# Kernel optimization log

Hardware: AMD Instinct MI355X
Metric: run time of the kernel (lower is better)

## Reference

```python
import jax, jax.numpy as jnp
import numpy as np

# Scaled-down LLaMA-style decoder with per-layer memory K/V prefix (tokenmix2 Decoder)
L, D, H, Dh, F, V = 2, 4096, 32, 128, 8192, 8192
B, S, M = 1, 1024, 512
EPS = 1e-5
ROPE_BASE = 10000.0


def setup_inputs() -> dict:
    key = jax.random.key(0)
    ks = jax.random.split(key, 16)
    sd = D ** -0.5
    sf = F ** -0.5
    n = lambda k, shape, s: (jax.random.normal(k, shape, jnp.float32) * s)
    return {
        "input_ids": jax.random.randint(ks[0], (B, S), 0, V),
        "memory": jax.random.normal(ks[1], (L, B, M, D), jnp.float32),
        "embed": n(ks[2], (V, D), sd),
        "Wq": n(ks[3], (L, D, D), sd),
        "Wk": n(ks[4], (L, D, D), sd),
        "Wv": n(ks[5], (L, D, D), sd),
        "Wo": n(ks[6], (L, D, D), sd),
        "Wg": n(ks[7], (L, F, D), sd),
        "Wu": n(ks[8], (L, F, D), sd),
        "Wd": n(ks[9], (L, D, F), sf),
        "Wmk": n(ks[10], (L, D, D), sd),
        "Wmv": n(ks[11], (L, D, D), sd),
        "ln1": jnp.ones((L, D), jnp.float32),
        "ln2": jnp.ones((L, D), jnp.float32),
        "normw": jnp.ones((D,), jnp.float32),
        "lm_head": n(ks[12], (V, D), sd),
    }


def _rms(x, w):
    return x * jax.lax.rsqrt(jnp.mean(x * x, axis=-1, keepdims=True) + EPS) * w


def _rot_half(x):
    x1, x2 = jnp.split(x, 2, axis=-1)
    return jnp.concatenate([-x2, x1], axis=-1)


def _rope_tables(n_pos):
    inv_freq = 1.0 / (ROPE_BASE ** (jnp.arange(0, Dh, 2, dtype=jnp.float32) / Dh))
    ang = jnp.arange(n_pos, dtype=jnp.float32)[:, None] * inv_freq[None, :]
    emb = jnp.concatenate([ang, ang], axis=-1)  # [n_pos, Dh]
    return jnp.cos(emb), jnp.sin(emb)


def reference(input_ids, memory, embed, Wq, Wk, Wv, Wo, Wg, Wu, Wd, Wmk, Wmv,
              ln1, ln2, normw, lm_head):
    h = embed[input_ids]                                   # [B,S,D]
    cos, sin = _rope_tables(M + S)                         # memory tokens sit at positions 0..M
    cos_k, sin_k = cos[None, None], sin[None, None]        # [1,1,M+S,Dh]
    cos_q, sin_q = cos[None, None, M:], sin[None, None, M:]  # queries at positions M..M+S
    qpos = jnp.arange(M, M + S)
    kpos = jnp.arange(M + S)
    mask = qpos[:, None] >= kpos[None, :]                  # causal incl. full memory prefix
    scale = Dh ** -0.5

    def heads(x, T):
        return x.reshape(B, T, H, Dh).transpose(0, 2, 1, 3)  # [B,H,T,Dh]

    for l in range(L):
        x = _rms(h, ln1[l])
        q = heads(x @ Wq[l].T, S)
        k = heads(x @ Wk[l].T, S)
        v = heads(x @ Wv[l].T, S)
        mk = heads(memory[l] @ Wmk[l].T, M)
        mv = heads(memory[l] @ Wmv[l].T, M)
        K = jnp.concatenate([mk, k], axis=2)               # [B,H,M+S,Dh]
        Vv = jnp.concatenate([mv, v], axis=2)
        q = q * cos_q + _rot_half(q) * sin_q
        K = K * cos_k + _rot_half(K) * sin_k
        scores = jnp.einsum('bhqd,bhkd->bhqk', q, K) * scale
        scores = jnp.where(mask, scores, jnp.float32(-1e30))
        p = jax.nn.softmax(scores, axis=-1)
        o = jnp.einsum('bhqk,bhkd->bhqd', p, Vv)
        o = o.transpose(0, 2, 1, 3).reshape(B, S, D)
        h = h + o @ Wo[l].T
        x = _rms(h, ln2[l])
        h = h + (jax.nn.silu(x @ Wg[l].T) * (x @ Wu[l].T)) @ Wd[l].T

    h = _rms(h, normw)
    logits = (h @ lm_head.T).astype(jnp.float32)           # [B,S,V]
    return logits
```

## Files before the change

kernel.cpp:

```cpp
#include <hip/hip_runtime.h>
#include <hip/hip_bf16.h>

typedef unsigned int uint;
typedef unsigned short u16;

#define D_ 4096
#define H_ 32
#define DH 128
#define F_ 8192
#define V_ 8192
#define S_ 1024
#define M_ 512
#define L_ 2
#define KV_ (M_ + S_)

typedef __attribute__((ext_vector_type(8))) short s16x8;
typedef __attribute__((ext_vector_type(4))) float f32x4;
typedef __attribute__((ext_vector_type(4))) u16 u16x4;

__device__ __forceinline__ u16 f2bf(float f) {
    uint u = __float_as_uint(f);
    u += 0x7FFFu + ((u >> 16) & 1u);
    return (u16)(u >> 16);
}
__device__ __forceinline__ float bf2f(u16 h) {
    return __uint_as_float(((uint)h) << 16);
}
__device__ __forceinline__ uint cvt_pk_bf16(float a, float b) {
    uint r;
    asm volatile("v_cvt_pk_bf16_f32 %0, %1, %2" : "=v"(r) : "v"(a), "v"(b));
    return r;
}
__device__ __forceinline__ void gload_lds16(const void* g, void* l) {
    __builtin_amdgcn_global_load_lds(
        (const __attribute__((address_space(1))) unsigned int*)g,
        (__attribute__((address_space(3))) unsigned int*)l, 16, 0, 0);
}

__global__ void k_embed(const int* __restrict__ ids, const float* __restrict__ embed,
                        float* __restrict__ h) {
    int row = blockIdx.x;
    const float4* src = (const float4*)(embed + (size_t)ids[row] * D_);
    float4* dst = (float4*)(h + (size_t)row * D_);
    for (int i = threadIdx.x; i < D_ / 4; i += 256) dst[i] = src[i];
}

__global__ __launch_bounds__(256) void k_rms(const float* __restrict__ hin,
                                             const float* __restrict__ w,
                                             u16* __restrict__ out) {
    int row = blockIdx.x, t = threadIdx.x;
    const float4* src = (const float4*)(hin + (size_t)row * D_);
    float4 v[4];
    float ss = 0.f;
#pragma unroll
    for (int i = 0; i < 4; ++i) {
        v[i] = src[t + 256 * i];
        ss += v[i].x * v[i].x + v[i].y * v[i].y + v[i].z * v[i].z + v[i].w * v[i].w;
    }
#pragma unroll
    for (int off = 32; off; off >>= 1) ss += __shfl_xor(ss, off);
    __shared__ float red[4];
    if ((t & 63) == 0) red[t >> 6] = ss;
    __syncthreads();
    float tot = red[0] + red[1] + red[2] + red[3];
    float sc = rsqrtf(tot * (1.0f / D_) + 1e-5f);
    const float4* wp = (const float4*)w;
    u16x4* op = (u16x4*)(out + (size_t)row * D_);
#pragma unroll
    for (int i = 0; i < 4; ++i) {
        float4 wv = wp[t + 256 * i];
        u16x4 o;
        o[0] = f2bf(v[i].x * sc * wv.x);
        o[1] = f2bf(v[i].y * sc * wv.y);
        o[2] = f2bf(v[i].z * sc * wv.z);
        o[3] = f2bf(v[i].w * sc * wv.w);
        op[t + 256 * i] = o;
    }
}

__global__ void k_cvt(const float* __restrict__ src, u16* __restrict__ dst, int n4) {
    int i = blockIdx.x * 256 + threadIdx.x;
    if (i < n4) {
        float4 v = ((const float4*)src)[i];
        u16x4 o;
        o[0] = f2bf(v.x); o[1] = f2bf(v.y); o[2] = f2bf(v.z); o[3] = f2bf(v.w);
        ((u16x4*)dst)[i] = o;
    }
}

__global__ void k_ropetab(float* __restrict__ tab) {
    int pos = blockIdx.x, i = threadIdx.x;
    float invf = powf(10000.0f, -(float)i * (1.0f / 64.0f));
    float ang = (float)pos * invf;
    tab[(size_t)pos * 128 + i * 2] = cosf(ang);
    tab[(size_t)pos * 128 + i * 2 + 1] = sinf(ang);
}

__global__ __launch_bounds__(256) void k_rope(u16* __restrict__ buf,
                                              const float* __restrict__ tab, int pos0) {
    int row = blockIdx.x, t = threadIdx.x;
    const float2* tp = (const float2*)(tab + (size_t)(pos0 + row) * 128);
    u16* p = buf + (size_t)row * D_;
#pragma unroll
    for (int j = 0; j < 8; ++j) {
        int pid = t + 256 * j;
        int hd = pid >> 6, i = pid & 63;
        float2 cs = tp[i];
        int base = hd * 128 + i;
        float v0 = bf2f(p[base]), v1 = bf2f(p[base + 64]);
        p[base] = f2bf(v0 * cs.x - v1 * cs.y);
        p[base + 64] = f2bf(v1 * cs.x + v0 * cs.y);
    }
}

__global__ __launch_bounds__(256) void k_transpose(const u16* __restrict__ src,
                                                   u16* __restrict__ dst) {
    __shared__ u16 tile[64][66];
    int tc = blockIdx.x * 64;
    int tr = blockIdx.y * 64;
    int t = threadIdx.x;
    int c = t & 63, r0 = t >> 6;
#pragma unroll
    for (int i = 0; i < 16; ++i) {
        int r = r0 + i * 4;
        tile[r][c] = src[(size_t)(tr + r) * D_ + tc + c];
    }
    __syncthreads();
#pragma unroll
    for (int i = 0; i < 16; ++i) {
        int r = r0 + i * 4;
        dst[(size_t)(tc + r) * KV_ + tr + c] = tile[c][r];
    }
}

struct GemmBatch {
    const u16* A[5];
    const float* B[5];
    void* O[5];
    int mrows[5];
    int koff[5];
    float* aux;
};

template <int EPI>
__global__ __launch_bounds__(256) void k_gemm(GemmBatch P, int Nn, int Kstep, int Kfull) {
    int z = blockIdx.z;
    size_t bm = blockIdx.y, bn = blockIdx.x;
    if ((int)(bm * 128) >= P.mrows[z]) return;
    const u16* A = P.A[z];
    const float* Bw = P.B[z];
    int koff = P.koff[z];

    __shared__ __align__(16) u16 As[128 * 64];
    __shared__ __align__(16) u16 Bs[128 * 64];
    int tid = threadIdx.x;
    int lane = tid & 63, wid = tid >> 6;
    int l16 = lane & 15, lh = lane >> 4;
    int wm = (wid >> 1) * 64, wn = (wid & 1) * 64;

    const u16* pA[4];
    const float* pB[4];
    int ldsAo[4], bso[4];
#pragma unroll
    for (int i = 0; i < 4; ++i) {
        int c = tid + 256 * i;
        int r = c >> 3, s = c & 7;
        pA[i] = A + (size_t)(bm * 128 + r) * Kfull + koff + s * 8;
        pB[i] = Bw + (size_t)(bn * 128 + r) * Kfull + koff + s * 8;
        ldsAo[i] = c * 8;
        bso[i] = r * 64 + ((s ^ (r & 7)) * 8);
    }

    f32x4 acc[4][4];
#pragma unroll
    for (int i = 0; i < 4; ++i)
#pragma unroll
        for (int j = 0; j < 4; ++j)
#pragma unroll
            for (int e = 0; e < 4; ++e) acc[i][j][e] = 0.f;

    float4 br[8];
    auto issueA = [&](int k0) {
#pragma unroll
        for (int i = 0; i < 4; ++i)
            gload_lds16(pA[i] + k0, &As[0] + ldsAo[i]);
    };
    auto loadB = [&](int k0) {
#pragma unroll
        for (int i = 0; i < 4; ++i) {
            br[2 * i] = *(const float4*)(pB[i] + k0);
            br[2 * i + 1] = *(const float4*)(pB[i] + k0 + 4);
        }
    };
    auto cvtwriteB = [&]() {
#pragma unroll
        for (int i = 0; i < 4; ++i) {
            uint4 w;
            w.x = cvt_pk_bf16(br[2 * i].x, br[2 * i].y);
            w.y = cvt_pk_bf16(br[2 * i].z, br[2 * i].w);
            w.z = cvt_pk_bf16(br[2 * i + 1].x, br[2 * i + 1].y);
            w.w = cvt_pk_bf16(br[2 * i + 1].z, br[2 * i + 1].w);
            *(uint4*)(&Bs[bso[i]]) = w;
        }
    };
    auto compute = [&]() {
#pragma unroll
        for (int kk = 0; kk < 2; ++kk) {
            int sidx = kk * 4 + lh;
            s16x8 af[4], bf4[4];
#pragma unroll
            for (int mi = 0; mi < 4; ++mi)
                af[mi] = *(const s16x8*)(&As[(wm + mi * 16 + l16) * 64 + sidx * 8]);
#pragma unroll
            for (int ni = 0; ni < 4; ++ni) {
                int r = wn + ni * 16 + l16;
                bf4[ni] = *(const s16x8*)(&Bs[r * 64 + ((sidx ^ (r & 7)) * 8)]);
            }
#pragma unroll
            for (int mi = 0; mi < 4; ++mi)
#pragma unroll
                for (int ni = 0; ni < 4; ++ni)
                    acc[mi][ni] = __builtin_amdgcn_mfma_f32_16x16x32_bf16(
                        af[mi], bf4[ni], acc[mi][ni], 0, 0, 0);
        }
    };

    int nt = Kstep >> 6;
    loadB(0);
    for (int t = 0; t < nt; ++t) {
        issueA(t << 6);
        cvtwriteB();
        if (t + 1 < nt) loadB((t + 1) << 6);
        __syncthreads();
        compute();
        __syncthreads();
    }

    void* Oo = P.O[z];
#pragma unroll
    for (int mi = 0; mi < 4; ++mi) {
#pragma unroll
        for (int ni = 0; ni < 4; ++ni) {
#pragma unroll
            for (int r = 0; r < 4; ++r) {
                int grow = (int)bm * 128 + wm + mi * 16 + lh * 4 + r;
                int gcol = (int)bn * 128 + wn + ni * 16 + l16;
                size_t idx = (size_t)grow * Nn + gcol;
                float v = acc[mi][ni][r];
                if constexpr (EPI == 0) {
                    ((u16*)Oo)[idx] = f2bf(v);
                } else if constexpr (EPI == 1) {
                    ((float*)Oo)[idx] = v;
                } else if constexpr (EPI == 3) {
                    float g = P.aux[idx];
                    float sg = g / (1.0f + __expf(-g));
                    ((u16*)Oo)[idx] = f2bf(sg * v);
                } else {
                    atomicAdd((float*)Oo + idx, v);
                }
            }
        }
    }
}

__global__ __launch_bounds__(64) void k_attn(const u16* __restrict__ Qb,
                                             const u16* __restrict__ Kb,
                                             const u16* __restrict__ VT,
                                             u16* __restrict__ Ob) {
    int qt = blockIdx.x, hd = blockIdx.y;
    int lane = threadIdx.x, l16 = lane & 15, lh = lane >> 4;
    __shared__ __align__(16) float Pl[16 * 36];

    s16x8 qf[4];
#pragma unroll
    for (int c = 0; c < 4; ++c)
        qf[c] = *(const s16x8*)(Qb + (size_t)(qt * 16 + l16) * D_ + hd * DH + c * 32 + lh * 8);

    f32x4 o[8];
#pragma unroll
    for (int dc = 0; dc < 8; ++dc)
#pragma unroll
        for (int e = 0; e < 4; ++e) o[dc][e] = 0.f;
    float m[4], lsum[4];
#pragma unroll
    for (int r = 0; r < 4; ++r) { m[r] = -1e30f; lsum[r] = 0.f; }

    const float scale = 0.08838834764831845f;
    int qbase = M_ + qt * 16;
    int nkb = (M_ + qt * 16 + 16 + 31) >> 5;

    for (int kb = 0; kb < nkb; ++kb) {
        f32x4 s0, s1;
#pragma unroll
        for (int e = 0; e < 4; ++e) { s0[e] = 0.f; s1[e] = 0.f; }
#pragma unroll
        for (int c = 0; c < 4; ++c) {
            s16x8 kf0 = *(const s16x8*)(Kb + (size_t)(kb * 32 + l16) * D_ + hd * DH + c * 32 + lh * 8);
            s16x8 kf1 = *(const s16x8*)(Kb + (size_t)(kb * 32 + 16 + l16) * D_ + hd * DH + c * 32 + lh * 8);
            s0 = __builtin_amdgcn_mfma_f32_16x16x32_bf16(qf[c], kf0, s0, 0, 0, 0);
            s1 = __builtin_amdgcn_mfma_f32_16x16x32_bf16(qf[c], kf1, s1, 0, 0, 0);
        }
        int kp0 = kb * 32 + l16, kp1 = kp0 + 16;
        float pm[4];
#pragma unroll
        for (int r = 0; r < 4; ++r) {
            int qp = qbase + lh * 4 + r;
            float v0 = s0[r] * scale; if (kp0 > qp) v0 = -1e30f;
            float v1 = s1[r] * scale; if (kp1 > qp) v1 = -1e30f;
            s0[r] = v0; s1[r] = v1;
            pm[r] = fmaxf(v0, v1);
        }
#pragma unroll
        for (int r = 0; r < 4; ++r) {
#pragma unroll
            for (int off = 8; off; off >>= 1) pm[r] = fmaxf(pm[r], __shfl_xor(pm[r], off));
        }
        float alpha[4];
#pragma unroll
        for (int r = 0; r < 4; ++r) {
            float mn = fmaxf(m[r], pm[r]);
            alpha[r] = __expf(m[r] - mn);
            m[r] = mn;
            float p0 = __expf(s0[r] - mn), p1 = __expf(s1[r] - mn);
            s0[r] = p0; s1[r] = p1;
            float t = p0 + p1;
#pragma unroll
            for (int off = 8; off; off >>= 1) t += __shfl_xor(t, off);
            lsum[r] = lsum[r] * alpha[r] + t;
        }
#pragma unroll
        for (int r = 0; r < 4; ++r) {
            Pl[(lh * 4 + r) * 36 + l16] = s0[r];
            Pl[(lh * 4 + r) * 36 + 16 + l16] = s1[r];
        }
        __syncthreads();
        s16x8 pf;
        {
            const f32x4* pp = (const f32x4*)(Pl + l16 * 36 + lh * 8);
            f32x4 a = pp[0], b = pp[1];
            pf[0] = (short)f2bf(a[0]); pf[1] = (short)f2bf(a[1]);
            pf[2] = (short)f2bf(a[2]); pf[3] = (short)f2bf(a[3]);
            pf[4] = (short)f2bf(b[0]); pf[5] = (short)f2bf(b[1]);
            pf[6] = (short)f2bf(b[2]); pf[7] = (short)f2bf(b[3]);
        }
        __syncthreads();
#pragma unroll
        for (int dc = 0; dc < 8; ++dc) {
#pragma unroll
            for (int r = 0; r < 4; ++r) o[dc][r] *= alpha[r];
        }
#pragma unroll
        for (int dc = 0; dc < 8; ++dc) {
            s16x8 vf = *(const s16x8*)(VT + (size_t)(hd * DH + dc * 16 + l16) * KV_ + kb * 32 + lh * 8);
            o[dc] = __builtin_amdgcn_mfma_f32_16x16x32_bf16(pf, vf, o[dc], 0, 0, 0);
        }
    }
#pragma unroll
    for (int dc = 0; dc < 8; ++dc) {
#pragma unroll
        for (int r = 0; r < 4; ++r) {
            float val = o[dc][r] / lsum[r];
            Ob[(size_t)(qt * 16 + lh * 4 + r) * D_ + hd * DH + dc * 16 + l16] = f2bf(val);
        }
    }
}

extern "C" void kernel_launch(void* const* d_in, const int* in_sizes, int n_in,
                              void* d_out, int out_size, void* d_ws, size_t ws_size,
                              hipStream_t stream) {
    const int* ids = (const int*)d_in[0];
    const float* memory = (const float*)d_in[1];
    const float* embed = (const float*)d_in[2];
    const float* Wq = (const float*)d_in[3];
    const float* Wk = (const float*)d_in[4];
    const float* Wv = (const float*)d_in[5];
    const float* Wo = (const float*)d_in[6];
    const float* Wg = (const float*)d_in[7];
    const float* Wu = (const float*)d_in[8];
    const float* Wd = (const float*)d_in[9];
    const float* Wmk = (const float*)d_in[10];
    const float* Wmv = (const float*)d_in[11];
    const float* ln1 = (const float*)d_in[12];
    const float* ln2 = (const float*)d_in[13];
    const float* normw = (const float*)d_in[14];
    const float* lm = (const float*)d_in[15];

    char* ws = (char*)d_ws;
    float* h   = (float*)(ws + 0x0000000);
    u16* xb    = (u16*)(ws + 0x1000000);
    float* tab = (float*)(ws + 0x1800000);
    u16* memb  = (u16*)(ws + 0x1900000);
    u16* Qb    = (u16*)(ws + 0x1E00000);
    u16* Kb    = (u16*)(ws + 0x2600000);
    u16* Vb    = (u16*)(ws + 0x3200000);
    u16* VT    = (u16*)(ws + 0x3E00000);
    u16* Ob    = (u16*)(ws + 0x4A00000);
    float* Gbuf = (float*)(ws + 0x1E00000);
    u16* tb     = (u16*)(ws + 0x3E00000);

    k_embed<<<S_, 256, 0, stream>>>(ids, embed, h);
    k_ropetab<<<KV_, 64, 0, stream>>>(tab);

    for (int l = 0; l < L_; ++l) {
        const float* Wq_l = Wq + (size_t)l * D_ * D_;
        const float* Wk_l = Wk + (size_t)l * D_ * D_;
        const float* Wv_l = Wv + (size_t)l * D_ * D_;
        const float* Wo_l = Wo + (size_t)l * D_ * D_;
        const float* Wmk_l = Wmk + (size_t)l * D_ * D_;
        const float* Wmv_l = Wmv + (size_t)l * D_ * D_;
        const float* Wg_l = Wg + (size_t)l * (size_t)F_ * D_;
        const float* Wu_l = Wu + (size_t)l * (size_t)F_ * D_;
        const float* Wd_l = Wd + (size_t)l * (size_t)D_ * F_;

        k_rms<<<S_, 256, 0, stream>>>(h, ln1 + l * D_, xb);
        k_cvt<<<(M_ * D_ / 4 + 255) / 256, 256, 0, stream>>>(
            memory + (size_t)l * M_ * D_, memb, M_ * D_ / 4);

        GemmBatch g1{};
        g1.A[0] = xb;   g1.B[0] = Wq_l;  g1.O[0] = Qb;                    g1.mrows[0] = S_;
        g1.A[1] = xb;   g1.B[1] = Wk_l;  g1.O[1] = Kb + (size_t)M_ * D_;  g1.mrows[1] = S_;
        g1.A[2] = xb;   g1.B[2] = Wv_l;  g1.O[2] = Vb + (size_t)M_ * D_;  g1.mrows[2] = S_;
        g1.A[3] = memb; g1.B[3] = Wmk_l; g1.O[3] = Kb;                    g1.mrows[3] = M_;
        g1.A[4] = memb; g1.B[4] = Wmv_l; g1.O[4] = Vb;                    g1.mrows[4] = M_;
        k_gemm<0><<<dim3(D_ / 128, S_ / 128, 5), 256, 0, stream>>>(g1, D_, D_, D_);

        k_rope<<<S_, 256, 0, stream>>>(Qb, tab, M_);
        k_rope<<<KV_, 256, 0, stream>>>(Kb, tab, 0);
        k_transpose<<<dim3(D_ / 64, KV_ / 64), 256, 0, stream>>>(Vb, VT);
        k_attn<<<dim3(S_ / 16, H_), 64, 0, stream>>>(Qb, Kb, VT, Ob);

        GemmBatch g2{};
        g2.A[0] = Ob; g2.B[0] = Wo_l; g2.O[0] = h; g2.mrows[0] = S_; g2.koff[0] = 0;
        g2.A[1] = Ob; g2.B[1] = Wo_l; g2.O[1] = h; g2.mrows[1] = S_; g2.koff[1] = 2048;
        k_gemm<4><<<dim3(D_ / 128, S_ / 128, 2), 256, 0, stream>>>(g2, D_, 2048, D_);

        k_rms<<<S_, 256, 0, stream>>>(h, ln2 + l * D_, xb);
        GemmBatch g3{};
        g3.A[0] = xb; g3.B[0] = Wg_l; g3.O[0] = Gbuf; g3.mrows[0] = S_;
        k_gemm<1><<<dim3(F_ / 128, S_ / 128, 1), 256, 0, stream>>>(g3, F_, D_, D_);
        GemmBatch g4{};
        g4.A[0] = xb; g4.B[0] = Wu_l; g4.O[0] = tb; g4.mrows[0] = S_; g4.aux = Gbuf;
        k_gemm<3><<<dim3(F_ / 128, S_ / 128, 1), 256, 0, stream>>>(g4, F_, D_, D_);
        GemmBatch g5{};
        g5.A[0] = tb; g5.B[0] = Wd_l; g5.O[0] = h; g5.mrows[0] = S_; g5.koff[0] = 0;
        g5.A[1] = tb; g5.B[1] = Wd_l; g5.O[1] = h; g5.mrows[1] = S_; g5.koff[1] = 4096;
        k_gemm<4><<<dim3(D_ / 128, S_ / 128, 2), 256, 0, stream>>>(g5, D_, 4096, F_);
    }

    k_rms<<<S_, 256, 0, stream>>>(h, normw, xb);
    GemmBatch g6{};
    g6.A[0] = xb; g6.B[0] = lm; g6.O[0] = (float*)d_out; g6.mrows[0] = S_;
    k_gemm<1><<<dim3(V_ / 128, S_ / 128, 1), 256, 0, stream>>>(g6, V_, D_, D_);
}
```

Baseline: 1.891 ms.

## Preconvert weights to bf16 and add pipelined 256x256 GEMM kernel

All fp32 weight matrices are converted to bf16 in workspace at the start of each call, so GEMMs load both operands directly into LDS with async loads instead of converting B tiles in registers. A new 512-thread 256x256 tile GEMM with double-buffered LDS, staggered prefetch and priority hints handles the QKV/memory projections and a batched gate/up projection. The SiLU epilogue moves to a separate elementwise kernel, and split-K atomic accumulation is replaced by single-pass read-add-write. This adds extra conversion traffic every call and drops the LDS swizzle, which may raise bank conflicts.

Measured after the change: 2.618 ms. 38.5% more time.

```diff
diff --git a/kernel.cpp b/kernel.cpp
--- a/kernel.cpp
+++ b/kernel.cpp
@@ -26,11 +26,6 @@
 __device__ __forceinline__ float bf2f(u16 h) {
     return __uint_as_float(((uint)h) << 16);
 }
-__device__ __forceinline__ uint cvt_pk_bf16(float a, float b) {
-    uint r;
-    asm volatile("v_cvt_pk_bf16_f32 %0, %1, %2" : "=v"(r) : "v"(a), "v"(b));
-    return r;
-}
 __device__ __forceinline__ void gload_lds16(const void* g, void* l) {
     __builtin_amdgcn_global_load_lds(
         (const __attribute__((address_space(1))) unsigned int*)g,
@@ -88,6 +83,21 @@
     }
 }
 
+__global__ void k_silu(const float* __restrict__ G, const float* __restrict__ U,
+                       u16* __restrict__ out, int n4) {
+    int i = blockIdx.x * 256 + threadIdx.x;
+    if (i < n4) {
+        float4 g = ((const float4*)G)[i];
+        float4 u = ((const float4*)U)[i];
+        u16x4 o;
+        o[0] = f2bf(g.x / (1.0f + __expf(-g.x)) * u.x);
+        o[1] = f2bf(g.y / (1.0f + __expf(-g.y)) * u.y);
+        o[2] = f2bf(g.z / (1.0f + __expf(-g.z)) * u.z);
+        o[3] = f2bf(g.w / (1.0f + __expf(-g.w)) * u.w);
+        ((u16x4*)out)[i] = o;
+    }
+}
+
 __global__ void k_ropetab(float* __restrict__ tab) {
     int pos = blockIdx.x, i = threadIdx.x;
     float invf = powf(10000.0f, -(float)i * (1.0f / 64.0f));
@@ -133,24 +143,138 @@
     }
 }
 
-struct GemmBatch {
+struct GemmB8 {
     const u16* A[5];
-    const float* B[5];
+    const u16* B[5];
     void* O[5];
     int mrows[5];
-    int koff[5];
-    float* aux;
 };
 
 template <int EPI>
-__global__ __launch_bounds__(256) void k_gemm(GemmBatch P, int Nn, int Kstep, int Kfull) {
+__global__ __launch_bounds__(512, 2) void k_gemm8(GemmB8 P, int Nn, int Kfull) {
+    int z = blockIdx.z;
+    size_t bm = blockIdx.y, bn = blockIdx.x;
+    if ((int)(bm * 256) >= P.mrows[z]) return;
+    const u16* A = P.A[z];
+    const u16* Bw = P.B[z];
+    __shared__ __align__(16) u16 AB[2][2][2][128][64];
+
+    const int tid = threadIdx.x;
+    const int lane = tid & 63, wid = tid >> 6;
+    const int l16 = lane & 15, lh = lane >> 4;
+    const int wrow = (wid >> 2) * 64;
+    const int wcol = (wid & 3) * 32;
+    const int nt = Kfull >> 6;
+
+    const int grow0 = tid >> 3;
+    const int gcol0 = (tid & 7) * 8;
+    const u16* pA = A + (size_t)(bm * 256 + grow0) * Kfull + gcol0;
+    const u16* pB = Bw + (size_t)(bn * 256 + grow0) * Kfull + gcol0;
+
+    auto stage = [&](const u16* base, int mat, int h, int t) {
+        if (t >= nt) return;
+        const u16* g = base + (size_t)(h * 128) * Kfull + t * 64;
+        u16* l = &AB[t & 1][mat][h][0][0] + tid * 8;
+        gload_lds16(g, l);
+        gload_lds16(g + (size_t)64 * Kfull, l + 4096);
+    };
+
+    f32x4 acc[4][4][2];
+#pragma unroll
+    for (int q = 0; q < 4; ++q)
+#pragma unroll
+        for (int mf = 0; mf < 4; ++mf)
+#pragma unroll
+            for (int nf = 0; nf < 2; ++nf)
+#pragma unroll
+                for (int e = 0; e < 4; ++e) acc[q][mf][nf][e] = 0.f;
+
+    stage(pA, 0, 0, 0); stage(pB, 1, 0, 0);
+    stage(pA, 0, 1, 0); stage(pB, 1, 1, 0);
+    stage(pA, 0, 0, 1); stage(pB, 1, 0, 1);
+    asm volatile("s_waitcnt vmcnt(4)" ::: "memory");
+    __builtin_amdgcn_s_barrier();
+    asm volatile("" ::: "memory");
+
+    for (int T = 0; T < nt; ++T) {
+        const int cb = T & 1;
+#pragma unroll
+        for (int q = 0; q < 4; ++q) {
+            const int qm = q >> 1, qn = q & 1;
+            s16x8 af[4][2], bb[2][2];
+#pragma unroll
+            for (int kk = 0; kk < 2; ++kk) {
+                const int co = (kk * 4 + lh) * 8;
+#pragma unroll
+                for (int mf = 0; mf < 4; ++mf)
+                    af[mf][kk] = *(const s16x8*)(&AB[cb][0][qm][wrow + mf * 16 + l16][co]);
+#pragma unroll
+                for (int nf = 0; nf < 2; ++nf)
+                    bb[nf][kk] = *(const s16x8*)(&AB[cb][1][qn][wcol + nf * 16 + l16][co]);
+            }
+            if (q == 0) stage(pA, 0, 1, T + 1);
+            else if (q == 1) stage(pB, 1, 1, T + 1);
+            else if (q == 2) stage(pA, 0, 0, T + 2);
+            else stage(pB, 1, 0, T + 2);
+            asm volatile("" ::: "memory");
+            __builtin_amdgcn_s_barrier();
+            asm volatile("" ::: "memory");
+            __builtin_amdgcn_s_setprio(1);
+#pragma unroll
+            for (int kk = 0; kk < 2; ++kk)
+#pragma unroll
+                for (int mf = 0; mf < 4; ++mf)
+#pragma unroll
+                    for (int nf = 0; nf < 2; ++nf)
+                        acc[q][mf][nf] = __builtin_amdgcn_mfma_f32_16x16x32_bf16(
+                            af[mf][kk], bb[nf][kk], acc[q][mf][nf], 0, 0, 0);
+            __builtin_amdgcn_s_setprio(0);
+            if (q == 3) {
+                if (T < nt - 2) asm volatile("s_waitcnt vmcnt(4)" ::: "memory");
+                else if (T == nt - 2) asm volatile("s_waitcnt vmcnt(0)" ::: "memory");
+            }
+            asm volatile("" ::: "memory");
+            __builtin_amdgcn_s_barrier();
+            asm volatile("" ::: "memory");
+        }
+    }
+
+    void* Oo = P.O[z];
+#pragma unroll
+    for (int q = 0; q < 4; ++q) {
+        const int qm = q >> 1, qn = q & 1;
+#pragma unroll
+        for (int mf = 0; mf < 4; ++mf) {
+#pragma unroll
+            for (int nf = 0; nf < 2; ++nf) {
+#pragma unroll
+                for (int rr = 0; rr < 4; ++rr) {
+                    int grow = (int)bm * 256 + qm * 128 + wrow + mf * 16 + lh * 4 + rr;
+                    int gcol = (int)bn * 256 + qn * 128 + wcol + nf * 16 + l16;
+                    size_t idx = (size_t)grow * Nn + gcol;
+                    float v = acc[q][mf][nf][rr];
+                    if constexpr (EPI == 0) ((u16*)Oo)[idx] = f2bf(v);
+                    else ((float*)Oo)[idx] = v;
+                }
+            }
+        }
+    }
+}
+
+struct GemmB2 {
+    const u16* A[5];
+    const u16* B[5];
+    void* O[5];
+    int mrows[5];
+};
+
+template <int EPI>
+__global__ __launch_bounds__(256) void k_gemm2(GemmB2 P, int Nn, int Kfull) {
     int z = blockIdx.z;
     size_t bm = blockIdx.y, bn = blockIdx.x;
     if ((int)(bm * 128) >= P.mrows[z]) return;
     const u16* A = P.A[z];
-    const float* Bw = P.B[z];
-    int koff = P.koff[z];
-
+    const u16* Bw = P.B[z];
     __shared__ __align__(16) u16 As[128 * 64];
     __shared__ __align__(16) u16 Bs[128 * 64];
     int tid = threadIdx.x;
@@ -158,17 +282,15 @@
     int l16 = lane & 15, lh = lane >> 4;
     int wm = (wid >> 1) * 64, wn = (wid & 1) * 64;
 
-    const u16* pA[4];
-    const float* pB[4];
-    int ldsAo[4], bso[4];
+    const u16 *pA[4], *pB[4];
+    int ldso[4];
 #pragma unroll
     for (int i = 0; i < 4; ++i) {
         int c = tid + 256 * i;
         int r = c >> 3, s = c & 7;
-        pA[i] = A + (size_t)(bm * 128 + r) * Kfull + koff + s * 8;
-        pB[i] = Bw + (size_t)(bn * 128 + r) * Kfull + koff + s * 8;
-        ldsAo[i] = c * 8;
-        bso[i] = r * 64 + ((s ^ (r & 7)) * 8);
+        pA[i] = A + (size_t)(bm * 128 + r) * Kfull + s * 8;
+        pB[i] = Bw + (size_t)(bn * 128 + r) * Kfull + s * 8;
+        ldso[i] = c * 8;
     }
 
     f32x4 acc[4][4];
@@ -179,31 +301,14 @@
 #pragma unroll
             for (int e = 0; e < 4; ++e) acc[i][j][e] = 0.f;
 
-    float4 br[8];
-    auto issueA = [&](int k0) {
-#pragma unroll
-        for (int i = 0; i < 4; ++i)
-            gload_lds16(pA[i] + k0, &As[0] + ldsAo[i]);
-    };
-    auto loadB = [&](int k0) {
-#pragma unroll
-        for (int i = 0; i < 4; ++i) {
-            br[2 * i] = *(const float4*)(pB[i] + k0);
-            br[2 * i + 1] = *(const float4*)(pB[i] + k0 + 4);
-        }
-    };
-    auto cvtwriteB = [&]() {
-#pragma unroll
-        for (int i = 0; i < 4; ++i) {
-            uint4 w;
-            w.x = cvt_pk_bf16(br[2 * i].x, br[2 * i].y);
-            w.y = cvt_pk_bf16(br[2 * i].z, br[2 * i].w);
-            w.z = cvt_pk_bf16(br[2 * i + 1].x, br[2 * i + 1].y);
-            w.w = cvt_pk_bf16(br[2 * i + 1].z, br[2 * i + 1].w);
-            *(uint4*)(&Bs[bso[i]]) = w;
-        }
-    };
-    auto compute = [&]() {
+    int nt = Kfull >> 6;
+    for (int t = 0; t < nt; ++t) {
+        int k0 = t << 6;
+#pragma unroll
+        for (int i = 0; i < 4; ++i) gload_lds16(pA[i] + k0, &As[ldso[i]]);
+#pragma unroll
+        for (int i = 0; i < 4; ++i) gload_lds16(pB[i] + k0, &Bs[ldso[i]]);
+        __syncthreads();
 #pragma unroll
         for (int kk = 0; kk < 2; ++kk) {
             int sidx = kk * 4 + lh;
@@ -212,10 +317,8 @@
             for (int mi = 0; mi < 4; ++mi)
                 af[mi] = *(const s16x8*)(&As[(wm + mi * 16 + l16) * 64 + sidx * 8]);
 #pragma unroll
-            for (int ni = 0; ni < 4; ++ni) {
-                int r = wn + ni * 16 + l16;
-                bf4[ni] = *(const s16x8*)(&Bs[r * 64 + ((sidx ^ (r & 7)) * 8)]);
-            }
+            for (int ni = 0; ni < 4; ++ni)
+                bf4[ni] = *(const s16x8*)(&Bs[(wn + ni * 16 + l16) * 64 + sidx * 8]);
 #pragma unroll
             for (int mi = 0; mi < 4; ++mi)
 #pragma unroll
@@ -223,16 +326,6 @@
                     acc[mi][ni] = __builtin_amdgcn_mfma_f32_16x16x32_bf16(
                         af[mi], bf4[ni], acc[mi][ni], 0, 0, 0);
         }
-    };
-
-    int nt = Kstep >> 6;
-    loadB(0);
-    for (int t = 0; t < nt; ++t) {
-        issueA(t << 6);
-        cvtwriteB();
-        if (t + 1 < nt) loadB((t + 1) << 6);
-        __syncthreads();
-        compute();
         __syncthreads();
     }
 
@@ -247,17 +340,8 @@
                 int gcol = (int)bn * 128 + wn + ni * 16 + l16;
                 size_t idx = (size_t)grow * Nn + gcol;
                 float v = acc[mi][ni][r];
-                if constexpr (EPI == 0) {
-                    ((u16*)Oo)[idx] = f2bf(v);
-                } else if constexpr (EPI == 1) {
-                    ((float*)Oo)[idx] = v;
-                } else if constexpr (EPI == 3) {
-                    float g = P.aux[idx];
-                    float sg = g / (1.0f + __expf(-g));
-                    ((u16*)Oo)[idx] = f2bf(sg * v);
-                } else {
-                    atomicAdd((float*)Oo + idx, v);
-                }
+                if constexpr (EPI == 1) ((float*)Oo)[idx] = v;
+                else ((float*)Oo)[idx] += v;
             }
         }
     }
@@ -397,58 +481,71 @@
     u16* Ob    = (u16*)(ws + 0x4A00000);
     float* Gbuf = (float*)(ws + 0x1E00000);
     u16* tb     = (u16*)(ws + 0x3E00000);
+    float* Ubuf = (float*)(ws + 0x4E00000);
+    u16* Wqb  = (u16*)(ws + 0x07000000);
+    u16* Wkb  = (u16*)(ws + 0x0B000000);
+    u16* Wvb  = (u16*)(ws + 0x0F000000);
+    u16* Wob  = (u16*)(ws + 0x13000000);
+    u16* Wmkb = (u16*)(ws + 0x17000000);
+    u16* Wmvb = (u16*)(ws + 0x1B000000);
+    u16* Wgb  = (u16*)(ws + 0x1F000000);
+    u16* Wub  = (u16*)(ws + 0x27000000);
+    u16* Wdb  = (u16*)(ws + 0x2F000000);
+    u16* lmb  = (u16*)(ws + 0x37000000);
+
+    const int nDD = L_ * D_ * D_ / 4, nFD = L_ * F_ * D_ / 4, nVD = V_ * D_ / 4;
+    k_cvt<<<(nDD + 255) / 256, 256, 0, stream>>>(Wq, Wqb, nDD);
+    k_cvt<<<(nDD + 255) / 256, 256, 0, stream>>>(Wk, Wkb, nDD);
+    k_cvt<<<(nDD + 255) / 256, 256, 0, stream>>>(Wv, Wvb, nDD);
+    k_cvt<<<(nDD + 255) / 256, 256, 0, stream>>>(Wo, Wob, nDD);
+    k_cvt<<<(nDD + 255) / 256, 256, 0, stream>>>(Wmk, Wmkb, nDD);
+    k_cvt<<<(nDD + 255) / 256, 256, 0, stream>>>(Wmv, Wmvb, nDD);
+    k_cvt<<<(nFD + 255) / 256, 256, 0, stream>>>(Wg, Wgb, nFD);
+    k_cvt<<<(nFD + 255) / 256, 256, 0, stream>>>(Wu, Wub, nFD);
+    k_cvt<<<(nFD + 255) / 256, 256, 0, stream>>>(Wd, Wdb, nFD);
+    k_cvt<<<(nVD + 255) / 256, 256, 0, stream>>>(lm, lmb, nVD);
 
     k_embed<<<S_, 256, 0, stream>>>(ids, embed, h);
     k_ropetab<<<KV_, 64, 0, stream>>>(tab);
 
     for (int l = 0; l < L_; ++l) {
-        const float* Wq_l = Wq + (size_t)l * D_ * D_;
-        const float* Wk_l = Wk + (size_t)l * D_ * D_;
-        const float* Wv_l = Wv + (size_t)l * D_ * D_;
-        const float* Wo_l = Wo + (size_t)l * D_ * D_;
-        const float* Wmk_l = Wmk + (size_t)l * D_ * D_;
-        const float* Wmv_l = Wmv + (size_t)l * D_ * D_;
-        const float* Wg_l = Wg + (size_t)l * (size_t)F_ * D_;
-        const float* Wu_l = Wu + (size_t)l * (size_t)F_ * D_;
-        const float* Wd_l = Wd + (size_t)l * (size_t)D_ * F_;
+        const size_t oDD = (size_t)l * D_ * D_;
+        const size_t oFD = (size_t)l * F_ * D_;
 
         k_rms<<<S_, 256, 0, stream>>>(h, ln1 + l * D_, xb);
         k_cvt<<<(M_ * D_ / 4 + 255) / 256, 256, 0, stream>>>(
             memory + (size_t)l * M_ * D_, memb, M_ * D_ / 4);
 
-        GemmBatch g1{};
-        g1.A[0] = xb;   g1.B[0] = Wq_l;  g1.O[0] = Qb;                    g1.mrows[0] = S_;
-        g1.A[1] = xb;   g1.B[1] = Wk_l;  g1.O[1] = Kb + (size_t)M_ * D_;  g1.mrows[1] = S_;
-        g1.A[2] = xb;   g1.B[2] = Wv_l;  g1.O[2] = Vb + (size_t)M_ * D_;  g1.mrows[2] = S_;
-        g1.A[3] = memb; g1.B[3] = Wmk_l; g1.O[3] = Kb;                    g1.mrows[3] = M_;
-        g1.A[4] = memb; g1.B[4] = Wmv_l; g1.O[4] = Vb;                    g1.mrows[4] = M_;
-        k_gemm<0><<<dim3(D_ / 128, S_ / 128, 5), 256, 0, stream>>>(g1, D_, D_, D_);
+        GemmB8 g1{};
+        g1.A[0] = xb;   g1.B[0] = Wqb + oDD;  g1.O[0] = Qb;                    g1.mrows[0] = S_;
+        g1.A[1] = xb;   g1.B[1] = Wkb + oDD;  g1.O[1] = Kb + (size_t)M_ * D_;  g1.mrows[1] = S_;
+        g1.A[2] = xb;   g1.B[2] = Wvb + oDD;  g1.O[2] = Vb + (size_t)M_ * D_;  g1.mrows[2] = S_;
+        g1.A[3] = memb; g1.B[3] = Wmkb + oDD; g1.O[3] = Kb;                    g1.mrows[3] = M_;
+        g1.A[4] = memb; g1.B[4] = Wmvb + oDD; g1.O[4] = Vb;                    g1.mrows[4] = M_;
+        k_gemm8<0><<<dim3(D_ / 256, S_ / 256, 5), 512, 0, stream>>>(g1, D_, D_);
 
         k_rope<<<S_, 256, 0, stream>>>(Qb, tab, M_);
         k_rope<<<KV_, 256, 0, stream>>>(Kb, tab, 0);
         k_transpose<<<dim3(D_ / 64, KV_ / 64), 256, 0, stream>>>(Vb, VT);
         k_attn<<<dim3(S_ / 16, H_), 64, 0, stream>>>(Qb, Kb, VT, Ob);
 
-        GemmBatch g2{};
-        g2.A[0] = Ob; g2.B[0] = Wo_l; g2.O[0] = h; g2.mrows[0] = S_; g2.koff[0] = 0;
-        g2.A[1] = Ob; g2.B[1] = Wo_l; g2.O[1] = h; g2.mrows[1] = S_; g2.koff[1] = 2048;
-        k_gemm<4><<<dim3(D_ / 128, S_ / 128, 2), 256, 0, stream>>>(g2, D_, 2048, D_);
+        GemmB2 g2{};
+        g2.A[0] = Ob; g2.B[0] = Wob + oDD; g2.O[0] = h; g2.mrows[0] = S_;
+        k_gemm2<2><<<dim3(D_ / 128, S_ / 128, 1), 256, 0, stream>>>(g2, D_, D_);
 
         k_rms<<<S_, 256, 0, stream>>>(h, ln2 + l * D_, xb);
-        GemmBatch g3{};
-        g3.A[0] = xb; g3.B[0] = Wg_l; g3.O[0] = Gbuf; g3.mrows[0] = S_;
-        k_gemm<1><<<dim3(F_ / 128, S_ / 128, 1), 256, 0, stream>>>(g3, F_, D_, D_);
-        GemmBatch g4{};
-        g4.A[0] = xb; g4.B[0] = Wu_l; g4.O[0] = tb; g4.mrows[0] = S_; g4.aux = Gbuf;
-        k_gemm<3><<<dim3(F_ / 128, S_ / 128, 1), 256, 0, stream>>>(g4, F_, D_, D_);
-        GemmBatch g5{};
-        g5.A[0] = tb; g5.B[0] = Wd_l; g5.O[0] = h; g5.mrows[0] = S_; g5.koff[0] = 0;
-        g5.A[1] = tb; g5.B[1] = Wd_l; g5.O[1] = h; g5.mrows[1] = S_; g5.koff[1] = 4096;
-        k_gemm<4><<<dim3(D_ / 128, S_ / 128, 2), 256, 0, stream>>>(g5, D_, 4096, F_);
+        GemmB8 g3{};
+        g3.A[0] = xb; g3.B[0] = Wgb + oFD; g3.O[0] = Gbuf; g3.mrows[0] = S_;
+        g3.A[1] = xb; g3.B[1] = Wub + oFD; g3.O[1] = Ubuf; g3.mrows[1] = S_;
+        k_gemm8<1><<<dim3(F_ / 256, S_ / 256, 2), 512, 0, stream>>>(g3, F_, D_);
+        k_silu<<<(S_ * F_ / 4 + 255) / 256, 256, 0, stream>>>(Gbuf, Ubuf, tb, S_ * F_ / 4);
+        GemmB2 g5{};
+        g5.A[0] = tb; g5.B[0] = Wdb + oFD; g5.O[0] = h; g5.mrows[0] = S_;
+        k_gemm2<2><<<dim3(D_ / 128, S_ / 128, 1), 256, 0, stream>>>(g5, D_, F_);
     }
 
     k_rms<<<S_, 256, 0, stream>>>(h, normw, xb);
-    GemmBatch g6{};
-    g6.A[0] = xb; g6.B[0] = lm; g6.O[0] = (float*)d_out; g6.mrows[0] = S_;
-    k_gemm<1><<<dim3(V_ / 128, S_ / 128, 1), 256, 0, stream>>>(g6, V_, D_, D_);
-}
+    GemmB2 g6{};
+    g6.A[0] = xb; g6.B[0] = lmb; g6.O[0] = (float*)d_out; g6.mrows[0] = S_;
+    k_gemm2<1><<<dim3(V_ / 128, S_ / 128, 1), 256, 0, stream>>>(g6, V_, D_);
+}
```
